# Optimization experiments

Hardware: AMD Instinct MI355X
Metric: run time of the kernel (lower is better)

Reference implementation:

```python
import jax, jax.numpy as jnp
import numpy as np

NV, NC, NI, D = 40000, 300, 7000, 128
NN = NV + NC + NI
E1 = E2 = 500000

def _l2norm(x, eps=1e-12):
    n = jnp.linalg.norm(x, axis=1, keepdims=True)
    return x / jnp.maximum(n, eps)

def _center_net(emb, idx, mask, dim_size, w1, b1, w2, b2):
    # Attention: MLP logits -> segment softmax over edges grouped by idx -> weighted segment sum
    h = jax.nn.relu(emb @ w1.T + b1)
    logits = h @ w2.T + b2                                  # [E, D], softmax per-column per-segment
    ml = jnp.where(mask[:, None], logits, -jnp.inf)
    m = jax.ops.segment_max(ml, idx, num_segments=dim_size)
    m = jnp.where(jnp.isfinite(m), m, 0.0)                  # empty segments
    e = jnp.where(mask[:, None], jnp.exp(logits - m[idx]), 0.0)
    den = jax.ops.segment_sum(e, idx, num_segments=dim_size)
    den = jnp.where(den > 0, den, 1.0)
    attn = e / den[idx]
    return jax.ops.segment_sum(attn * emb, idx, num_segments=dim_size)

def _offset_net(off, idx, mask, dim_size):
    # scatter_max over masked edges; torch_scatter leaves empty segments at 0
    src = jnp.where(mask[:, None], jax.nn.relu(off), -jnp.inf)
    m = jax.ops.segment_max(src, idx, num_segments=dim_size)
    return jnp.maximum(m, 0.0)

def _forward(vc, vo, cc, co, ic, io, vt, aw1, ab1, aw2, ab2, tw1, tb1, tw2, tb2, g1, g2):
    all_center = jnp.concatenate([vc, cc, ic], axis=0)      # [NN, D]
    all_offset = jax.nn.relu(jnp.concatenate([vo, co, io], axis=0))
    h1, t1 = g1[0], g1[1]
    full = jnp.ones(h1.shape, bool)
    agg1 = _center_net(all_center[t1], h1, full, NN, aw1, ab1, aw2, ab2)[:NV]
    agg1 = _l2norm(agg1)
    off1 = all_offset[t1]
    m_iv1 = (h1 < NV) & (t1 >= NV) & (t1 < NV + NC)
    iv_off1 = _offset_net(off1, h1, m_iv1, NN)[:NV]
    m_ui1 = (h1 < NV) & (t1 >= NV + NC)
    ut_off1 = _offset_net(off1, h1, m_ui1, NN)[:NV]
    h2, t2 = g2[0], g2[1]
    m_ev = (h2 < NV) & (t2 >= NV)
    agg_emb1 = _center_net(all_center[t2], h2, m_ev, NV, aw1, ab1, aw2, ab2)
    tinv = (1.0 / vt)[:, None]                              # [NV, 1]
    ta = jax.nn.relu(tinv @ tw1.T + tb1)
    te = jax.nn.softmax(ta @ tw2.T + tb2, axis=0)
    agg_emb2 = agg_emb1 * te
    m_vv = (h2 < NV) & (t2 < NV)
    t2c = jnp.where(m_vv, t2, 0)                            # safe gather for masked edges
    agg2 = _l2norm(_center_net(agg_emb2[t2c], h2, m_vv, NV, aw1, ab1, aw2, ab2))
    lam = 1.0
    visit_final_emb = lam * agg1 + (1.0 - lam) * agg2
    off2 = all_offset[t2]
    m_iv2 = (h2 < NV) & (t2 >= NV) & (t2 < NV + NC)
    iv_off2 = _offset_net(off2, h2, m_iv2, NN)[:NV]
    m_ui2 = (h2 < NV) & (t2 >= NV + NC)
    ut_off2 = _offset_net(off2, h2, m_ui2, NN)[:NV]
    vv_off = _offset_net(off2, h2, m_vv, NV)
    # scatter_max over visit_union_idx == elementwise max of the 5 [NV,D] blocks
    stack = jnp.stack([iv_off1, ut_off1, iv_off2, ut_off2, vv_off], axis=0)
    visit_final_offset = jax.nn.relu(jnp.max(stack, axis=0))
    return visit_final_emb, visit_final_offset

def setup_inputs() -> dict:
    key = jax.random.key(0)
    ks = jax.random.split(key, 16)
    f = lambda i, s: jax.random.normal(ks[i], s, jnp.float32)
    return {
        "visit_center": f(0, (NV, D)), "visit_offset": f(1, (NV, D)),
        "ccs_center": f(2, (NC, D)), "ccs_offset": f(3, (NC, D)),
        "icd_center": f(4, (NI, D)), "icd_offset": f(5, (NI, D)),
        "visit_time": jax.random.uniform(ks[6], (NV,), jnp.float32) + 1.0,
        "aw1": f(7, (D, D)) * 0.08, "ab1": jnp.zeros((D,), jnp.float32),
        "aw2": f(8, (D, D)) * 0.08, "ab2": jnp.zeros((D,), jnp.float32),
        "tw1": f(9, (1, 1)), "tb1": jnp.zeros((1,), jnp.float32),
        "tw2": f(10, (1, 1)), "tb2": jnp.zeros((1,), jnp.float32),
        "graph1_idx": jax.random.randint(ks[11], (2, E1), 0, NN),
        "graph2_idx": jax.random.randint(ks[12], (2, E2), 0, NN),
    }

def reference(visit_center, visit_offset, ccs_center, ccs_offset, icd_center, icd_offset, visit_time, aw1, ab1, aw2, ab2, tw1, tb1, tw2, tb2, graph1_idx, graph2_idx):
    return _forward(visit_center, visit_offset, ccs_center, ccs_offset, icd_center, icd_offset,
                    visit_time, aw1, ab1, aw2, ab2, tw1, tb1, tw2, tb2, graph1_idx, graph2_idx)
```

## Files before the change

kernel.cpp:

```cpp
#include <hip/hip_runtime.h>
#include <cstdint>

#define NVv 40000
#define NCc 300
#define NIi 7000
#define NNn 47300
#define DD 128
#define E1N 500000
#define E2N 500000

#define CAP 48
#define NSEC (3 * NVv)
#define NSEC8 (NSEC / 8)
#define MLPB ((NNn + 127) / 128)
#define SCB ((E1N + E2N + 1023) / 1024)
#define WBLK 32
#define OB16 ((NNn * 16 + 255) / 256)
#define SEGB ((NVv + 3) / 4)

typedef __attribute__((ext_vector_type(8))) short short8v;
typedef __attribute__((ext_vector_type(4))) short short4v;
typedef __attribute__((ext_vector_type(4))) float f32x4;
typedef __attribute__((ext_vector_type(2))) float f32x2;

__device__ __forceinline__ short f2bf(float f) {
    unsigned u = __float_as_uint(f);
    u += 0x7FFF + ((u >> 16) & 1);
    return (short)(u >> 16);
}
__device__ __forceinline__ float bf2f(short s) {
    return __uint_as_float(((unsigned)(unsigned short)s) << 16);
}

#if __has_builtin(__builtin_amdgcn_cvt_pk_f32_fp8) && __has_builtin(__builtin_amdgcn_cvt_pk_fp8_f32)
#define HWFP8 1
#else
#define HWFP8 0
#endif

__device__ __forceinline__ unsigned f2fp8_sw(float f) {
    unsigned u = __float_as_uint(f);
    unsigned s = (u >> 24) & 0x80u;
    float a = fabsf(f);
    if (!(a >= 0.015625f)) return s;
    a = fminf(a, 448.f);
    unsigned au = __float_as_uint(a);
    au += 0x7FFFFu + ((au >> 20) & 1);
    int ee = (int)(au >> 23) - 120;
    unsigned mm = (au >> 20) & 7u;
    return s | ((unsigned)ee << 3) | mm;
}
__device__ __forceinline__ float fp82f_sw(unsigned b) {
    unsigned s = (b & 0x80u) << 24;
    unsigned ex = (b >> 3) & 0xFu, mm = b & 7u;
    if (ex == 0) {
        float v = (float)mm * 0.001953125f;
        return (b & 0x80u) ? -v : v;
    }
    return __uint_as_float(s | ((ex + 120u) << 23) | (mm << 20));
}
__device__ __forceinline__ f32x2 dec2lo(unsigned u) {
#if HWFP8
    auto r = __builtin_amdgcn_cvt_pk_f32_fp8((int)u, false);
    f32x2 o; o.x = r[0]; o.y = r[1]; return o;
#else
    f32x2 o; o.x = fp82f_sw(u & 0xffu); o.y = fp82f_sw((u >> 8) & 0xffu); return o;
#endif
}
__device__ __forceinline__ f32x2 dec2hi(unsigned u) {
#if HWFP8
    auto r = __builtin_amdgcn_cvt_pk_f32_fp8((int)u, true);
    f32x2 o; o.x = r[0]; o.y = r[1]; return o;
#else
    f32x2 o; o.x = fp82f_sw((u >> 16) & 0xffu); o.y = fp82f_sw((u >> 24) & 0xffu); return o;
#endif
}
__device__ __forceinline__ unsigned enc4(float a, float b, float c, float d) {
#if HWFP8
    int r = __builtin_amdgcn_cvt_pk_fp8_f32(a, b, 0, false);
    r = __builtin_amdgcn_cvt_pk_fp8_f32(c, d, r, true);
    return (unsigned)r;
#else
    return f2fp8_sw(a) | (f2fp8_sw(b) << 8) | (f2fp8_sw(c) << 16) | (f2fp8_sw(d) << 24);
#endif
}

__device__ __forceinline__ const float* node_row(const float* __restrict__ v,
                                                 const float* __restrict__ c,
                                                 const float* __restrict__ i, int t) {
    return t < NVv ? v + (size_t)t * DD
         : t < NVv + NCc ? c + (size_t)(t - NVv) * DD
                         : i + (size_t)(t - NVv - NCc) * DD;
}

__global__ void prep(const int* __restrict__ g1, const int* __restrict__ g2,
                     int* __restrict__ cnt, unsigned short* __restrict__ csr,
                     const float* __restrict__ w1, const float* __restrict__ w2,
                     short* __restrict__ Wbf,
                     const float* __restrict__ vo, const float* __restrict__ co,
                     const float* __restrict__ io,
                     unsigned char* __restrict__ TC, short* __restrict__ O) {
    int bid = blockIdx.x;
    if (bid < 8 * SCB) {
        int cls = bid & 7;
        int c4 = (bid >> 3) * 1024 + threadIdx.x * 4;
        if (c4 >= E1N + E2N) return;
        bool isg1 = c4 < E1N;
        const int* gg = isg1 ? g1 : g2;
        int off = isg1 ? c4 : c4 - E1N;
        int4 hv = *(const int4*)(gg + off);
        int hs[4] = {hv.x, hv.y, hv.z, hv.w};
        #pragma unroll
        for (int i = 0; i < 4; ++i) {
            int h = hs[i];
            if (h >= NVv || (h & 7) != cls) continue;
            int t = gg[E1N + off + i];
            int sr;
            if (isg1) sr = cls * NSEC8 + (t >= NVv ? (h >> 3) : 5000 + (h >> 3));
            else      sr = cls * NSEC8 + 10000 + (h >> 3);
            int idx = atomicAdd(cnt + sr, 1);
            if (idx < CAP) csr[sr * CAP + idx] = (unsigned short)t;
        }
        return;
    }
    if (bid < 8 * SCB + OB16) {
        int gid = (bid - 8 * SCB) * 256 + threadIdx.x;
        int n = gid >> 4, l = gid & 15;
        if (n >= NNn) return;
        const float* orow = node_row(vo, co, io, n);
        float4 x = *(const float4*)(orow + 8 * l);
        float4 y = *(const float4*)(orow + 8 * l + 4);
        short8v s;
        s[0] = f2bf(x.x); s[1] = f2bf(x.y); s[2] = f2bf(x.z); s[3] = f2bf(x.w);
        s[4] = f2bf(y.x); s[5] = f2bf(y.y); s[6] = f2bf(y.z); s[7] = f2bf(y.w);
        *(short8v*)(O + (size_t)n * 128 + 8 * l) = s;
        return;
    }
    if (bid < 8 * SCB + OB16 + WBLK) {
        int e = (bid - 8 * SCB - OB16) * 1024 + threadIdx.x * 4;
        float4 v = e < DD * DD ? *(const float4*)(w1 + e)
                               : *(const float4*)(w2 + e - DD * DD);
        short4v s;
        s.x = f2bf(v.x); s.y = f2bf(v.y); s.z = f2bf(v.z); s.w = f2bf(v.w);
        *(short4v*)(Wbf + e) = s;
        return;
    }
    int t = threadIdx.x;
    if (t < 64) ((int*)(TC + (size_t)NNn * 256))[t] = 0;
    else if (t < 128) ((int*)(O + (size_t)NNn * 128))[t - 64] = 0;
}

__global__ __launch_bounds__(256, 2) void node_mlp(
        const float* __restrict__ vc, const float* __restrict__ cc,
        const float* __restrict__ ic,
        const short* __restrict__ Wbf,
        const float* __restrict__ b1, const float* __restrict__ b2,
        unsigned char* __restrict__ TC) {
    __shared__ short hbuf[128][136];
    const int tid = threadIdx.x;
    const int lane = tid & 63, wv = tid >> 6;
    const int n0b = blockIdx.x * 128;
    const int colw = lane & 15;
    const int k0 = (lane >> 4) * 8;
    const int rrow = (lane >> 4) * 4;

    short8v a[2][4];
    #pragma unroll
    for (int t = 0; t < 2; ++t) {
        int arow = n0b + wv * 32 + t * 16 + colw;
        if (arow >= NNn) arow = NNn - 1;
        const float* ar = node_row(vc, cc, ic, arow);
        #pragma unroll
        for (int kf = 0; kf < 4; ++kf) {
            const float* p = ar + kf * 32 + k0;
            float4 x = *(const float4*)p;
            float4 y = *(const float4*)(p + 4);
            short8v f;
            f[0] = f2bf(x.x); f[1] = f2bf(x.y); f[2] = f2bf(x.z); f[3] = f2bf(x.w);
            f[4] = f2bf(y.x); f[5] = f2bf(y.y); f[6] = f2bf(y.z); f[7] = f2bf(y.w);
            a[t][kf] = f;
        }
    }

    #pragma unroll
    for (int hf = 0; hf < 2; ++hf) {
        short8v bw[4][4];
        #pragma unroll
        for (int jj = 0; jj < 4; ++jj)
            #pragma unroll
            for (int kf = 0; kf < 4; ++kf)
                bw[jj][kf] = *(const short8v*)
                    (Wbf + ((hf * 4 + jj) * 16 + colw) * DD + kf * 32 + k0);
        #pragma unroll
        for (int jj = 0; jj < 4; ++jj) {
            int j = (hf * 4 + jj) * 16 + colw;
            float bb = b1[j];
            f32x4 ac0 = {bb, bb, bb, bb}, ac1 = ac0;
            #pragma unroll
            for (int kf = 0; kf < 4; ++kf) {
                ac0 = __builtin_amdgcn_mfma_f32_16x16x32_bf16(a[0][kf], bw[jj][kf], ac0, 0, 0, 0);
                ac1 = __builtin_amdgcn_mfma_f32_16x16x32_bf16(a[1][kf], bw[jj][kf], ac1, 0, 0, 0);
            }
            #pragma unroll
            for (int r = 0; r < 4; ++r) {
                hbuf[wv * 32 + rrow + r][j] = f2bf(fmaxf(ac0[r], 0.f));
                hbuf[wv * 32 + 16 + rrow + r][j] = f2bf(fmaxf(ac1[r], 0.f));
            }
        }
    }

    short8v a2[2][4];
    #pragma unroll
    for (int t = 0; t < 2; ++t)
        #pragma unroll
        for (int kf = 0; kf < 4; ++kf)
            a2[t][kf] = *(short8v*)&hbuf[wv * 32 + t * 16 + colw][kf * 32 + k0];

    #pragma unroll
    for (int hf = 0; hf < 2; ++hf) {
        short8v bw[4][4];
        #pragma unroll
        for (int jj = 0; jj < 4; ++jj)
            #pragma unroll
            for (int kf = 0; kf < 4; ++kf)
                bw[jj][kf] = *(const short8v*)
                    (Wbf + DD * DD + ((hf * 4 + jj) * 16 + colw) * DD + kf * 32 + k0);
        #pragma unroll
        for (int jj = 0; jj < 4; ++jj) {
            int j = (hf * 4 + jj) * 16 + colw;
            float bb = b2[j];
            f32x4 ac0 = {bb, bb, bb, bb}, ac1 = ac0;
            #pragma unroll
            for (int kf = 0; kf < 4; ++kf) {
                ac0 = __builtin_amdgcn_mfma_f32_16x16x32_bf16(a2[0][kf], bw[jj][kf], ac0, 0, 0, 0);
                ac1 = __builtin_amdgcn_mfma_f32_16x16x32_bf16(a2[1][kf], bw[jj][kf], ac1, 0, 0, 0);
            }
            #pragma unroll
            for (int r = 0; r < 4; ++r) {
                hbuf[wv * 32 + rrow + r][j] = f2bf(__expf(ac0[r]));
                hbuf[wv * 32 + 16 + rrow + r][j] = f2bf(__expf(ac1[r]));
            }
        }
    }
    __syncthreads();

    #pragma unroll
    for (int i = 0; i < 8; ++i) {
        int cid = i * 256 + tid;
        int r = cid >> 4, p = cid & 15;
        int n = n0b + r;
        if (n >= NNn) continue;
        const float* cr = node_row(vc, cc, ic, n);
        float4 c0 = *(const float4*)(cr + 8 * p);
        float4 c1 = *(const float4*)(cr + 8 * p + 4);
        short8v el = *(const short8v*)&hbuf[r][8 * p];
        uint4 s;
        s.x = enc4(bf2f(el[0]), bf2f(el[1]), bf2f(el[2]), bf2f(el[3]));
        s.y = enc4(bf2f(el[4]), bf2f(el[5]), bf2f(el[6]), bf2f(el[7]));
        s.z = enc4(c0.x, c0.y, c0.z, c0.w);
        s.w = enc4(c1.x, c1.y, c1.z, c1.w);
        *(uint4*)(TC + (size_t)n * 256 + 16 * p) = s;
    }
}

__device__ __forceinline__ void accTC(uint4 a, float d[8], float n[8]) {
    f32x2 e01 = dec2lo(a.x), e23 = dec2hi(a.x), e45 = dec2lo(a.y), e67 = dec2hi(a.y);
    f32x2 c01 = dec2lo(a.z), c23 = dec2hi(a.z), c45 = dec2lo(a.w), c67 = dec2hi(a.w);
    d[0] += e01.x; n[0] = fmaf(e01.x, c01.x, n[0]);
    d[1] += e01.y; n[1] = fmaf(e01.y, c01.y, n[1]);
    d[2] += e23.x; n[2] = fmaf(e23.x, c23.x, n[2]);
    d[3] += e23.y; n[3] = fmaf(e23.y, c23.y, n[3]);
    d[4] += e45.x; n[4] = fmaf(e45.x, c45.x, n[4]);
    d[5] += e45.y; n[5] = fmaf(e45.y, c45.y, n[5]);
    d[6] += e67.x; n[6] = fmaf(e67.x, c67.x, n[6]);
    d[7] += e67.y; n[7] = fmaf(e67.y, c67.y, n[7]);
}
__device__ __forceinline__ void accO(short8v o, float m[8]) {
    #pragma unroll
    for (int j = 0; j < 8; ++j) m[j] = fmaxf(m[j], bf2f(o[j]));
}

__global__ void seg_fused(const int* __restrict__ cnt,
                          const unsigned short* __restrict__ csr,
                          const unsigned char* __restrict__ TC,
                          const short* __restrict__ O,
                          float* __restrict__ out0, float* __restrict__ out1) {
    int seg = blockIdx.x * 4 + (threadIdx.x >> 6);
    if (seg >= NVv) return;
    int lane = threadIdx.x & 63;
    int quarter = lane >> 4, q = lane & 15;
    int sbase = (seg & 7) * NSEC8 + (seg >> 3);
    float d[8] = {0,0,0,0,0,0,0,0};
    float n[8] = {0,0,0,0,0,0,0,0};
    float m[8] = {0,0,0,0,0,0,0,0};

    {
        int len = cnt[sbase]; if (len > CAP) len = CAP;
        int tl = (lane < len) ? (int)csr[sbase * CAP + lane] : NNn;
        for (int k = 0; k < len; k += 16) {
            uint4 a[4]; short8v o[4];
            #pragma unroll
            for (int u = 0; u < 4; ++u) {
                int t = __shfl(tl, k + 4 * u + quarter);
                a[u] = *(const uint4*)(TC + ((size_t)t << 8) + 16 * q);
                o[u] = *(const short8v*)(O + ((size_t)t << 7) + 8 * q);
            }
            #pragma unroll
            for (int u = 0; u < 4; ++u) { accTC(a[u], d, n); accO(o[u], m); }
        }
    }
    {
        int sr = sbase + 5000;
        int len = cnt[sr]; if (len > CAP) len = CAP;
        int tl = (lane < len) ? (int)csr[sr * CAP + lane] : NNn;
        for (int k = 0; k < len; k += 16) {
            uint4 a[4];
            #pragma unroll
            for (int u = 0; u < 4; ++u) {
                int t = __shfl(tl, k + 4 * u + quarter);
                a[u] = *(const uint4*)(TC + ((size_t)t << 8) + 16 * q);
            }
            #pragma unroll
            for (int u = 0; u < 4; ++u) accTC(a[u], d, n);
        }
    }
    {
        int sr = sbase + 10000;
        int len = cnt[sr]; if (len > CAP) len = CAP;
        int tl = (lane < len) ? (int)csr[sr * CAP + lane] : NNn;
        for (int k = 0; k < len; k += 16) {
            short8v o[4];
            #pragma unroll
            for (int u = 0; u < 4; ++u) {
                int t = __shfl(tl, k + 4 * u + quarter);
                o[u] = *(const short8v*)(O + ((size_t)t << 7) + 8 * q);
            }
            #pragma unroll
            for (int u = 0; u < 4; ++u) accO(o[u], m);
        }
    }

    #pragma unroll
    for (int j = 0; j < 8; ++j) {
        d[j] += __shfl_xor(d[j], 16); d[j] += __shfl_xor(d[j], 32);
        n[j] += __shfl_xor(n[j], 16); n[j] += __shfl_xor(n[j], 32);
        m[j] = fmaxf(m[j], __shfl_xor(m[j], 16));
        m[j] = fmaxf(m[j], __shfl_xor(m[j], 32));
    }
    float v[8], ss = 0.f;
    #pragma unroll
    for (int j = 0; j < 8; ++j) {
        v[j] = d[j] > 0.f ? n[j] / d[j] : 0.f;
        ss += v[j] * v[j];
    }
    #pragma unroll
    for (int off = 8; off; off >>= 1) ss += __shfl_xor(ss, off);
    float inv = 1.f / fmaxf(sqrtf(ss), 1e-12f);
    size_t b = (size_t)seg * DD + 8 * q;
    if (quarter == 0) {
        *(float4*)(out0 + b) = make_float4(v[0]*inv, v[1]*inv, v[2]*inv, v[3]*inv);
        *(float4*)(out0 + b + 4) = make_float4(v[4]*inv, v[5]*inv, v[6]*inv, v[7]*inv);
    } else if (quarter == 1) {
        *(float4*)(out1 + b) = make_float4(m[0], m[1], m[2], m[3]);
        *(float4*)(out1 + b + 4) = make_float4(m[4], m[5], m[6], m[7]);
    }
}

extern "C" void kernel_launch(void* const* d_in, const int* in_sizes, int n_in,
                              void* d_out, int out_size, void* d_ws, size_t ws_size,
                              hipStream_t stream) {
    const float* vc  = (const float*)d_in[0];
    const float* vo  = (const float*)d_in[1];
    const float* cc  = (const float*)d_in[2];
    const float* co  = (const float*)d_in[3];
    const float* ic  = (const float*)d_in[4];
    const float* io  = (const float*)d_in[5];
    const float* aw1 = (const float*)d_in[7];
    const float* ab1 = (const float*)d_in[8];
    const float* aw2 = (const float*)d_in[9];
    const float* ab2 = (const float*)d_in[10];
    const int*   g1  = (const int*)d_in[15];
    const int*   g2  = (const int*)d_in[16];

    float* out0 = (float*)d_out;
    float* out1 = out0 + (size_t)NVv * DD;

    unsigned char* TC = (unsigned char*)d_ws;
    short* O   = (short*)(TC + (size_t)(NNn + 1) * 256);
    int* cnt   = (int*)(O + (size_t)(NNn + 1) * 128);
    short* Wbf = (short*)(cnt + NSEC);
    unsigned short* csr = (unsigned short*)(Wbf + 2 * DD * DD);

    hipMemsetAsync(cnt, 0, NSEC * sizeof(int), stream);

    prep<<<8 * SCB + OB16 + WBLK + 1, 256, 0, stream>>>(
        g1, g2, cnt, csr, aw1, aw2, Wbf, vo, co, io, TC, O);
    node_mlp<<<MLPB, 256, 0, stream>>>(vc, cc, ic, Wbf, ab1, ab2, TC);
    seg_fused<<<SEGB, 256, 0, stream>>>(cnt, csr, TC, O, out0, out1);
}
```

Measured before the change: 143.2 us.

## Interleave TC row as 8-byte chunks and split segment waves into halves

The packed exp/center row layout changes from 16-byte chunks of 8 channels to 8-byte chunks of 4 channels. The segment-reduction kernel now has each wave process 2 edges per step with 32 lanes each, instead of 4 edges with 16 lanes each. The aim is to cut per-lane registers and the cross-quarter shuffle reductions. In exchange, loads are narrower (8-byte instead of 16-byte), so more memory instructions and more shuffles per edge are needed for the gathered rows.

```diff
diff --git a/kernel.cpp b/kernel.cpp
--- a/kernel.cpp
+++ b/kernel.cpp
@@ -245,39 +245,34 @@
     __syncthreads();
 
     #pragma unroll
-    for (int i = 0; i < 8; ++i) {
+    for (int i = 0; i < 16; ++i) {
         int cid = i * 256 + tid;
-        int r = cid >> 4, p = cid & 15;
+        int r = cid >> 5, p = cid & 31;
         int n = n0b + r;
         if (n >= NNn) continue;
         const float* cr = node_row(vc, cc, ic, n);
-        float4 c0 = *(const float4*)(cr + 8 * p);
-        float4 c1 = *(const float4*)(cr + 8 * p + 4);
-        short8v el = *(const short8v*)&hbuf[r][8 * p];
-        uint4 s;
-        s.x = enc4(bf2f(el[0]), bf2f(el[1]), bf2f(el[2]), bf2f(el[3]));
-        s.y = enc4(bf2f(el[4]), bf2f(el[5]), bf2f(el[6]), bf2f(el[7]));
-        s.z = enc4(c0.x, c0.y, c0.z, c0.w);
-        s.w = enc4(c1.x, c1.y, c1.z, c1.w);
-        *(uint4*)(TC + (size_t)n * 256 + 16 * p) = s;
-    }
-}
-
-__device__ __forceinline__ void accTC(uint4 a, float d[8], float n[8]) {
-    f32x2 e01 = dec2lo(a.x), e23 = dec2hi(a.x), e45 = dec2lo(a.y), e67 = dec2hi(a.y);
-    f32x2 c01 = dec2lo(a.z), c23 = dec2hi(a.z), c45 = dec2lo(a.w), c67 = dec2hi(a.w);
+        float4 cv = *(const float4*)(cr + 4 * p);
+        short4v el = *(const short4v*)&hbuf[r][4 * p];
+        uint2 s;
+        s.x = enc4(bf2f(el.x), bf2f(el.y), bf2f(el.z), bf2f(el.w));
+        s.y = enc4(cv.x, cv.y, cv.z, cv.w);
+        *(uint2*)(TC + (size_t)n * 256 + 8 * p) = s;
+    }
+}
+
+__device__ __forceinline__ void accTC(uint2 a, float d[4], float n[4]) {
+    f32x2 e01 = dec2lo(a.x), e23 = dec2hi(a.x);
+    f32x2 c01 = dec2lo(a.y), c23 = dec2hi(a.y);
     d[0] += e01.x; n[0] = fmaf(e01.x, c01.x, n[0]);
     d[1] += e01.y; n[1] = fmaf(e01.y, c01.y, n[1]);
     d[2] += e23.x; n[2] = fmaf(e23.x, c23.x, n[2]);
     d[3] += e23.y; n[3] = fmaf(e23.y, c23.y, n[3]);
-    d[4] += e45.x; n[4] = fmaf(e45.x, c45.x, n[4]);
-    d[5] += e45.y; n[5] = fmaf(e45.y, c45.y, n[5]);
-    d[6] += e67.x; n[6] = fmaf(e67.x, c67.x, n[6]);
-    d[7] += e67.y; n[7] = fmaf(e67.y, c67.y, n[7]);
-}
-__device__ __forceinline__ void accO(short8v o, float m[8]) {
-    #pragma unroll
-    for (int j = 0; j < 8; ++j) m[j] = fmaxf(m[j], bf2f(o[j]));
+}
+__device__ __forceinline__ void acc4(short4v o, float m[4]) {
+    m[0] = fmaxf(m[0], bf2f(o.x));
+    m[1] = fmaxf(m[1], bf2f(o.y));
+    m[2] = fmaxf(m[2], bf2f(o.z));
+    m[3] = fmaxf(m[3], bf2f(o.w));
 }
 
 __global__ void seg_fused(const int* __restrict__ cnt,
@@ -288,37 +283,37 @@
     int seg = blockIdx.x * 4 + (threadIdx.x >> 6);
     if (seg >= NVv) return;
     int lane = threadIdx.x & 63;
-    int quarter = lane >> 4, q = lane & 15;
+    int half = lane >> 5, q = lane & 31;
     int sbase = (seg & 7) * NSEC8 + (seg >> 3);
-    float d[8] = {0,0,0,0,0,0,0,0};
-    float n[8] = {0,0,0,0,0,0,0,0};
-    float m[8] = {0,0,0,0,0,0,0,0};
+    float d[4] = {0,0,0,0};
+    float n[4] = {0,0,0,0};
+    float m[4] = {0,0,0,0};
 
     {
         int len = cnt[sbase]; if (len > CAP) len = CAP;
         int tl = (lane < len) ? (int)csr[sbase * CAP + lane] : NNn;
-        for (int k = 0; k < len; k += 16) {
-            uint4 a[4]; short8v o[4];
+        for (int k = 0; k < len; k += 8) {
+            uint2 a[4]; short4v o[4];
             #pragma unroll
             for (int u = 0; u < 4; ++u) {
-                int t = __shfl(tl, k + 4 * u + quarter);
-                a[u] = *(const uint4*)(TC + ((size_t)t << 8) + 16 * q);
-                o[u] = *(const short8v*)(O + ((size_t)t << 7) + 8 * q);
-            }
-            #pragma unroll
-            for (int u = 0; u < 4; ++u) { accTC(a[u], d, n); accO(o[u], m); }
+                int t = __shfl(tl, k + 2 * u + half);
+                a[u] = *(const uint2*)(TC + ((size_t)t << 8) + 8 * q);
+                o[u] = *(const short4v*)(O + ((size_t)t << 7) + 4 * q);
+            }
+            #pragma unroll
+            for (int u = 0; u < 4; ++u) { accTC(a[u], d, n); acc4(o[u], m); }
         }
     }
     {
         int sr = sbase + 5000;
         int len = cnt[sr]; if (len > CAP) len = CAP;
         int tl = (lane < len) ? (int)csr[sr * CAP + lane] : NNn;
-        for (int k = 0; k < len; k += 16) {
-            uint4 a[4];
+        for (int k = 0; k < len; k += 8) {
+            uint2 a[4];
             #pragma unroll
             for (int u = 0; u < 4; ++u) {
-                int t = __shfl(tl, k + 4 * u + quarter);
-                a[u] = *(const uint4*)(TC + ((size_t)t << 8) + 16 * q);
+                int t = __shfl(tl, k + 2 * u + half);
+                a[u] = *(const uint2*)(TC + ((size_t)t << 8) + 8 * q);
             }
             #pragma unroll
             for (int u = 0; u < 4; ++u) accTC(a[u], d, n);
@@ -328,42 +323,38 @@
         int sr = sbase + 10000;
         int len = cnt[sr]; if (len > CAP) len = CAP;
         int tl = (lane < len) ? (int)csr[sr * CAP + lane] : NNn;
-        for (int k = 0; k < len; k += 16) {
-            short8v o[4];
+        for (int k = 0; k < len; k += 8) {
+            short4v o[4];
             #pragma unroll
             for (int u = 0; u < 4; ++u) {
-                int t = __shfl(tl, k + 4 * u + quarter);
-                o[u] = *(const short8v*)(O + ((size_t)t << 7) + 8 * q);
-            }
-            #pragma unroll
-            for (int u = 0; u < 4; ++u) accO(o[u], m);
-        }
-    }
-
-    #pragma unroll
-    for (int j = 0; j < 8; ++j) {
-        d[j] += __shfl_xor(d[j], 16); d[j] += __shfl_xor(d[j], 32);
-        n[j] += __shfl_xor(n[j], 16); n[j] += __shfl_xor(n[j], 32);
-        m[j] = fmaxf(m[j], __shfl_xor(m[j], 16));
+                int t = __shfl(tl, k + 2 * u + half);
+                o[u] = *(const short4v*)(O + ((size_t)t << 7) + 4 * q);
+            }
+            #pragma unroll
+            for (int u = 0; u < 4; ++u) acc4(o[u], m);
+        }
+    }
+
+    #pragma unroll
+    for (int j = 0; j < 4; ++j) {
+        d[j] += __shfl_xor(d[j], 32);
+        n[j] += __shfl_xor(n[j], 32);
         m[j] = fmaxf(m[j], __shfl_xor(m[j], 32));
     }
-    float v[8], ss = 0.f;
-    #pragma unroll
-    for (int j = 0; j < 8; ++j) {
+    float v[4], ss = 0.f;
+    #pragma unroll
+    for (int j = 0; j < 4; ++j) {
         v[j] = d[j] > 0.f ? n[j] / d[j] : 0.f;
         ss += v[j] * v[j];
     }
     #pragma unroll
-    for (int off = 8; off; off >>= 1) ss += __shfl_xor(ss, off);
+    for (int off = 16; off; off >>= 1) ss += __shfl_xor(ss, off);
     float inv = 1.f / fmaxf(sqrtf(ss), 1e-12f);
-    size_t b = (size_t)seg * DD + 8 * q;
-    if (quarter == 0) {
+    size_t b = (size_t)seg * DD + 4 * q;
+    if (half == 0)
         *(float4*)(out0 + b) = make_float4(v[0]*inv, v[1]*inv, v[2]*inv, v[3]*inv);
-        *(float4*)(out0 + b + 4) = make_float4(v[4]*inv, v[5]*inv, v[6]*inv, v[7]*inv);
-    } else if (quarter == 1) {
+    else
         *(float4*)(out1 + b) = make_float4(m[0], m[1], m[2], m[3]);
-        *(float4*)(out1 + b + 4) = make_float4(m[4], m[5], m[6], m[7]);
-    }
 }
 
 extern "C" void kernel_launch(void* const* d_in, const int* in_sizes, int n_in,
```

Result: faster. 125.2 us (-12.6%).
